# Kernel tuning notes

Measured on AMD Instinct MI355X. Metric: run time of the kernel, lower is better.

Reference implementation:

```python
import jax, jax.numpy as jnp
import numpy as np

EMBED_DIM = 1024
N_HEADS = 16

def setup_inputs() -> dict:
    key = jax.random.key(0)
    ks = jax.random.split(key, 5)
    C = EMBED_DIM
    std = 1.0 / np.sqrt(C)
    x = jax.random.normal(ks[0], (2, 2048, C), dtype=jnp.float32)
    w_attn = jax.random.normal(ks[1], (C, 3 * C), dtype=jnp.float32) * std  # (in, out)
    b_attn = jax.random.normal(ks[2], (3 * C,), dtype=jnp.float32) * 0.01
    w_proj = jax.random.normal(ks[3], (C, C), dtype=jnp.float32) * std
    b_proj = jax.random.normal(ks[4], (C,), dtype=jnp.float32) * 0.01
    return {"x": x, "w_attn": w_attn, "b_attn": b_attn, "w_proj": w_proj, "b_proj": b_proj}

def reference(x, w_attn, b_attn, w_proj, b_proj):
    B, T, C = x.shape
    H = N_HEADS
    D = C // H
    qkv = x @ w_attn + b_attn                      # (B, T, 3C)
    q, k, v = jnp.split(qkv, 3, axis=2)
    # (B, T, C) -> (B, H, T, D)
    q = q.reshape(B, T, H, D).transpose(0, 2, 1, 3)
    k = k.reshape(B, T, H, D).transpose(0, 2, 1, 3)
    v = v.reshape(B, T, H, D).transpose(0, 2, 1, 3)
    # Faithful to source: query is divided by scale BEFORE QK^T, and the
    # similarity is divided by scale AGAIN before softmax (net scale = 1/D).
    scale = jnp.asarray(D, dtype=x.dtype) ** 0.5
    q = q / scale
    sim = jnp.einsum('bhnd,bhsd->bhns', q, k)      # (B, H, T, T)
    causal = jnp.tril(jnp.ones((T, T), dtype=bool))
    neg_min = jnp.finfo(sim.dtype).min
    sim = jnp.where(causal[None, None, :, :], sim, neg_min)
    attn = jax.nn.softmax(sim / scale, axis=-1)
    out = jnp.einsum('bhns,bhsd->bhnd', attn, v)   # (B, H, T, D)
    # source: gqa returns (b n h d), forward does transpose(1,2) -> (b h n d)
    # then .view(B, T, C); net effect is reshaping the (B,H,T,D) layout.
    y = out.reshape(B, T, C)
    y = y @ w_proj + b_proj
    return y
```

## Files before the change

### kernel.cpp

```cpp
#include <hip/hip_runtime.h>
#include <hip/hip_bf16.h>

#define BB 2
#define TT 2048
#define CC 1024
#define HH 16
#define DD 64
#define MM (BB*TT)
#define QSZ ((size_t)MM*CC)

#define QSCALE 0.022542110013890053f

typedef __attribute__((ext_vector_type(8))) short bf16x8;
typedef __attribute__((ext_vector_type(4))) float f32x4;
typedef __attribute__((address_space(1))) const unsigned char as1_u8;
typedef __attribute__((address_space(3))) unsigned char as3_u8;

struct alignas(8) bf16x4_s { __hip_bfloat16 h[4]; };

static __device__ __forceinline__ unsigned cvt_pk_bf16(float lo, float hi) {
    unsigned r;
    asm("v_cvt_pk_bf16_f32 %0, %1, %2" : "=v"(r) : "v"(lo), "v"(hi));
    return r;
}

__constant__ unsigned char U_qi[48] = {
    15,31,30,31, 14,29,30,28,29, 13,27,28,26,27, 12,25,26,24,25,
    11,23,24,22,23, 10,21,22,20,21, 9,19,20,18,19, 8,17,18,16,17,
    7,16, 6,5,4,3,2,1,0};
__constant__ unsigned char U_t0[48] = {
    0,0,15,16, 0,0,0,14,15, 0,0,0,13,14, 0,0,0,12,13,
    0,0,0,11,12, 0,0,0,10,11, 0,0,0,9,10, 0,0,0,8,9,
    0,0, 0,0,0,0,0,0,0};
__constant__ unsigned char U_t1[48] = {
    16,16,31,32, 15,15,15,29,30, 14,14,14,27,28, 13,13,13,25,26,
    12,12,12,23,24, 11,11,11,21,22, 10,10,10,19,20, 9,9,9,17,18,
    8,8, 7,6,5,4,3,2,1};

__global__ __launch_bounds__(256) void prep_kernel(
    const float* __restrict__ x,  __hip_bfloat16* __restrict__ xb,
    const float* __restrict__ wa, __hip_bfloat16* __restrict__ wqkvT,
    const float* __restrict__ wp, __hip_bfloat16* __restrict__ wprojT)
{
    __shared__ float tile[64][68];
    const int t = threadIdx.x;
    const int b = blockIdx.x;
    if (b < 2048) {
        const int i = (b * 256 + t) * 8;
        const float4 a = *(const float4*)&x[i];
        const float4 c = *(const float4*)&x[i + 4];
        uint2 lo, hi;
        lo.x = cvt_pk_bf16(a.x, a.y); lo.y = cvt_pk_bf16(a.z, a.w);
        hi.x = cvt_pk_bf16(c.x, c.y); hi.y = cvt_pk_bf16(c.z, c.w);
        *(uint2*)&xb[i] = lo;
        *(uint2*)&xb[i + 4] = hi;
        return;
    }
    const float* in; __hip_bfloat16* outp; int R, Cc, bx, by;
    if (b < 2816) { const int i = b - 2048; in = wa; outp = wqkvT; R = CC; Cc = 3*CC; bx = i % 48; by = i / 48; }
    else          { const int i = b - 2816; in = wp; outp = wprojT; R = CC; Cc = CC;  bx = i % 16; by = i / 16; }
    const int c0 = bx * 64, r0 = by * 64;
    {
        const int r = t >> 2, cb = (t & 3) * 16;
        #pragma unroll
        for (int i = 0; i < 4; ++i)
            *(float4*)&tile[r][cb + i*4] = *(const float4*)&in[(size_t)(r0 + r)*Cc + c0 + cb + i*4];
    }
    __syncthreads();
    {
        const int c = t >> 2, rb = (t & 3) * 16;
        uint2 o0, o1;
        o0.x = cvt_pk_bf16(tile[rb+0][c],  tile[rb+1][c]);
        o0.y = cvt_pk_bf16(tile[rb+2][c],  tile[rb+3][c]);
        o1.x = cvt_pk_bf16(tile[rb+4][c],  tile[rb+5][c]);
        o1.y = cvt_pk_bf16(tile[rb+6][c],  tile[rb+7][c]);
        __hip_bfloat16* dst = outp + (size_t)(c0 + c)*R + r0 + rb;
        *(uint2*)&dst[0] = o0; *(uint2*)&dst[4] = o1;
        o0.x = cvt_pk_bf16(tile[rb+8][c],  tile[rb+9][c]);
        o0.y = cvt_pk_bf16(tile[rb+10][c], tile[rb+11][c]);
        o1.x = cvt_pk_bf16(tile[rb+12][c], tile[rb+13][c]);
        o1.y = cvt_pk_bf16(tile[rb+14][c], tile[rb+15][c]);
        *(uint2*)&dst[8] = o0; *(uint2*)&dst[12] = o1;
    }
}

template<int MODE>
__global__ __launch_bounds__(256) void gemm_mfma(
    const __hip_bfloat16* __restrict__ A,
    const __hip_bfloat16* __restrict__ BT,
    const float* __restrict__ bias,
    void* __restrict__ out, int M, int N, int K)
{
    __shared__ __hip_bfloat16 As[128][64];
    __shared__ __hip_bfloat16 Bs[128][64];

    const int tid = threadIdx.x;
    const int w = tid >> 6, l = tid & 63;
    const int lr = l & 15, lg = l >> 4;
    const int wr = w >> 1, wc = w & 1;
    const int rsw = (lr & 7) << 4;
    const int lsw = ((l & 7) ^ (l >> 3)) * 8;

    const int nwg = gridDim.x * gridDim.y;
    const int bid = blockIdx.y * gridDim.x + blockIdx.x;
    const int swz_id = (bid & 7) * (nwg >> 3) + (bid >> 3);
    const int row0 = (swz_id / gridDim.x) * 128;
    const int col0 = (swz_id % gridDim.x) * 128;

    f32x4 acc[4][4] = {};

    for (int k0 = 0; k0 < K; k0 += 64) {
        __syncthreads();
        #pragma unroll
        for (int i = 0; i < 4; ++i) {
            const int br = w*32 + i*8;
            const __hip_bfloat16* ga = A  + (size_t)(row0 + br + (l>>3))*K + k0 + lsw;
            __builtin_amdgcn_global_load_lds((as1_u8*)ga, (as3_u8*)&As[br][0], 16, 0, 0);
            const __hip_bfloat16* gb = BT + (size_t)(col0 + br + (l>>3))*K + k0 + lsw;
            __builtin_amdgcn_global_load_lds((as1_u8*)gb, (as3_u8*)&Bs[br][0], 16, 0, 0);
        }
        __syncthreads();

        #pragma unroll
        for (int s = 0; s < 2; ++s) {
            bf16x8 af[4], bfr[4];
            #pragma unroll
            for (int m = 0; m < 4; ++m) {
                const char* ab = (const char*)&As[wr*64 + m*16 + lr][0];
                af[m] = *(const bf16x8*)(ab + ((s*64 + lg*16) ^ rsw));
            }
            #pragma unroll
            for (int n = 0; n < 4; ++n) {
                const char* bb = (const char*)&Bs[wc*64 + n*16 + lr][0];
                bfr[n] = *(const bf16x8*)(bb + ((s*64 + lg*16) ^ rsw));
            }
            #pragma unroll
            for (int m = 0; m < 4; ++m)
                #pragma unroll
                for (int n = 0; n < 4; ++n)
                    acc[m][n] = __builtin_amdgcn_mfma_f32_16x16x32_bf16(af[m], bfr[n], acc[m][n], 0, 0, 0);
        }
    }

    #pragma unroll
    for (int m = 0; m < 4; ++m) {
        #pragma unroll
        for (int n = 0; n < 4; ++n) {
            const int ng = col0 + wc*64 + n*16 + lr;
            const float bv = bias[ng];
            const int mg0 = row0 + wr*64 + m*16 + lg*4;
            if (MODE == 0) {
                const int which = ng >> 10, c = ng & 1023;
                const int h = c >> 6, d = c & 63;
                if (which == 2) {
                    const int b = mg0 >> 11, t0 = mg0 & 2047;
                    uint2 pv;
                    pv.x = cvt_pk_bf16(acc[m][n][0] + bv, acc[m][n][1] + bv);
                    pv.y = cvt_pk_bf16(acc[m][n][2] + bv, acc[m][n][3] + bv);
                    *(uint2*)((__hip_bfloat16*)out + (size_t)2*QSZ +
                        (((size_t)(b*HH + h))*DD + d)*TT + t0) = pv;
                } else {
                    #pragma unroll
                    for (int r = 0; r < 4; ++r) {
                        const int mg = mg0 + r;
                        float v = acc[m][n][r] + bv;
                        if (which == 0) v *= QSCALE;
                        const int b = mg >> 11, t = mg & 2047;
                        ((__hip_bfloat16*)out)[(size_t)which*QSZ +
                            (((size_t)(b*HH + h))*TT + t)*DD + d] = __float2bfloat16(v);
                    }
                }
            } else {
                #pragma unroll
                for (int r = 0; r < 4; ++r)
                    ((float*)out)[(size_t)(mg0 + r)*N + ng] = acc[m][n][r] + bv;
            }
        }
    }
}

__global__ __launch_bounds__(256) void attn_mfma(
    const __hip_bfloat16* __restrict__ Qb,
    const __hip_bfloat16* __restrict__ Kb,
    const __hip_bfloat16* __restrict__ Vb,
    __hip_bfloat16* __restrict__ Ob,
    __hip_bfloat16* __restrict__ Opart,
    float* __restrict__ Lpart)
{
    __shared__ __hip_bfloat16 k_lds[64][64];
    __shared__ __hip_bfloat16 vT[64][64];
    __shared__ __hip_bfloat16 p_lds[4][16][64];

    const int tid = threadIdx.x;
    const int w  = tid >> 6;
    const int l  = tid & 63;
    const int lr = l & 15;
    const int lg = l >> 4;
    const int swz = (lr & 7) << 4;

    const int bid = blockIdx.x;
    const int sid = (bid & 7) * 192 + (bid >> 3);
    const int bh  = sid / 48;
    const int u   = sid % 48;
    const int qi  = U_qi[u];
    const int t0i = U_t0[u];
    const int t1i = U_t1[u];
    const int qb  = qi * 64;

    const __hip_bfloat16* Qh = Qb + (size_t)bh*TT*DD;
    const __hip_bfloat16* Kh = Kb + (size_t)bh*TT*DD;
    const __hip_bfloat16* Vh = Vb + (size_t)bh*DD*TT;

    bf16x8 qa[2];
    const int qrow = qb + w*16 + lr;
    {
        const __hip_bfloat16* qp = Qh + (size_t)qrow*DD + lg*8;
        qa[0] = *(const bf16x8*)(qp);
        qa[1] = *(const bf16x8*)(qp + 32);
    }

    const int off0 = (16*lg) ^ swz;
    const int off1 = (64 + 16*lg) ^ swz;
    const char* kr0b = (const char*)&k_lds[lr][0];
    const char* vr0b = (const char*)&vT[lr][0];
    char* pwb = (char*)&p_lds[w][lr][0];
    int pwo[4];
    #pragma unroll
    for (int mt = 0; mt < 4; ++mt) pwo[mt] = (32*mt + 8*lg) ^ swz;

    const int srow = tid >> 2, sch = tid & 3;
    const int wswz = (srow & 7) << 4;
    char* kwr = (char*)&k_lds[srow][0];
    char* vwr = (char*)&vT[srow][0];
    const int wo0 = (sch*32) ^ wswz, wo1 = (sch*32 + 16) ^ wswz;

    const __hip_bfloat16* ksrc = Kh + (size_t)(t0i*64 + srow)*DD + sch*16;
    const __hip_bfloat16* vsrc = Vh + (size_t)srow*TT + t0i*64 + sch*16;

    float4 kr0 = *(const float4*)ksrc, kr1 = *(const float4*)(ksrc + 8);
    float4 vr0 = *(const float4*)vsrc, vr1 = *(const float4*)(vsrc + 8);
    ksrc += 64*DD; vsrc += 64;
    *(float4*)(kwr + wo0) = kr0; *(float4*)(kwr + wo1) = kr1;
    *(float4*)(vwr + wo0) = vr0; *(float4*)(vwr + wo1) = vr1;
    __syncthreads();

    f32x4 oacc[4] = {};
    f32x4 lacc = {0.f, 0.f, 0.f, 0.f};

    for (int t = t0i; t < t1i; ++t) {
        const int kv0 = t * 64;
        const bool has_next = (t + 1 < t1i);

        if (has_next) {
            kr0 = *(const float4*)ksrc; kr1 = *(const float4*)(ksrc + 8);
            vr0 = *(const float4*)vsrc; vr1 = *(const float4*)(vsrc + 8);
            ksrc += 64*DD; vsrc += 64;
        }

        f32x4 sacc[4] = {};
        __builtin_amdgcn_s_setprio(1);
        #pragma unroll
        for (int mt = 0; mt < 4; ++mt) {
            const bf16x8 kb0 = *(const bf16x8*)(kr0b + mt*2048 + off0);
            const bf16x8 kb1 = *(const bf16x8*)(kr0b + mt*2048 + off1);
            sacc[mt] = __builtin_amdgcn_mfma_f32_16x16x32_bf16(kb0, qa[0], sacc[mt], 0, 0, 0);
            sacc[mt] = __builtin_amdgcn_mfma_f32_16x16x32_bf16(kb1, qa[1], sacc[mt], 0, 0, 0);
        }
        __builtin_amdgcn_s_setprio(0);

        if (t == qi) {
            #pragma unroll
            for (int mt = 0; mt < 4; ++mt)
                #pragma unroll
                for (int r = 0; r < 4; ++r)
                    if (kv0 + mt*16 + lg*4 + r > qrow) sacc[mt][r] = -3.0e38f;
        }
        #pragma unroll
        for (int mt = 0; mt < 4; ++mt) {
            const float p0 = exp2f(sacc[mt][0]), p1 = exp2f(sacc[mt][1]);
            const float p2 = exp2f(sacc[mt][2]), p3 = exp2f(sacc[mt][3]);
            lacc[mt] += (p0 + p1) + (p2 + p3);
            uint2 pp;
            pp.x = cvt_pk_bf16(p0, p1);
            pp.y = cvt_pk_bf16(p2, p3);
            *(uint2*)(pwb + pwo[mt]) = pp;
        }

        const bf16x8 pb0 = *(const bf16x8*)(pwb + off0);
        const bf16x8 pb1 = *(const bf16x8*)(pwb + off1);
        __builtin_amdgcn_s_setprio(1);
        #pragma unroll
        for (int dt = 0; dt < 4; ++dt) {
            const bf16x8 vb0 = *(const bf16x8*)(vr0b + dt*2048 + off0);
            const bf16x8 vb1 = *(const bf16x8*)(vr0b + dt*2048 + off1);
            oacc[dt] = __builtin_amdgcn_mfma_f32_16x16x32_bf16(vb0, pb0, oacc[dt], 0, 0, 0);
            oacc[dt] = __builtin_amdgcn_mfma_f32_16x16x32_bf16(vb1, pb1, oacc[dt], 0, 0, 0);
        }
        __builtin_amdgcn_s_setprio(0);

        if (has_next) {
            __syncthreads();
            *(float4*)(kwr + wo0) = kr0; *(float4*)(kwr + wo1) = kr1;
            *(float4*)(vwr + wo0) = vr0; *(float4*)(vwr + wo1) = vr1;
            __syncthreads();
        }
    }

    float l_r = (lacc[0] + lacc[1]) + (lacc[2] + lacc[3]);
    l_r += __shfl_xor(l_r, 16);
    l_r += __shfl_xor(l_r, 32);

    if (qi >= 16) {
        const int s = (t0i != 0);
        const int unit = ((bh*16 + (qi - 16)) << 1) | s;
        const int rowu = w*16 + lr;
        __hip_bfloat16* Oprow = Opart + ((size_t)unit*64 + rowu)*64;
        #pragma unroll
        for (int dt = 0; dt < 4; ++dt) {
            uint2 ov;
            ov.x = cvt_pk_bf16(oacc[dt][0], oacc[dt][1]);
            ov.y = cvt_pk_bf16(oacc[dt][2], oacc[dt][3]);
            *(uint2*)(Oprow + dt*16 + lg*4) = ov;
        }
        if (lg == 0) Lpart[unit*64 + rowu] = l_r;
    } else {
        __hip_bfloat16* Orow = Ob + ((size_t)bh*TT + qrow)*DD;
        const float inv = 1.0f / l_r;
        #pragma unroll
        for (int dt = 0; dt < 4; ++dt) {
            uint2 ov;
            ov.x = cvt_pk_bf16(oacc[dt][0]*inv, oacc[dt][1]*inv);
            ov.y = cvt_pk_bf16(oacc[dt][2]*inv, oacc[dt][3]*inv);
            *(uint2*)(Orow + dt*16 + lg*4) = ov;
        }
    }
}

__global__ __launch_bounds__(256) void attn_combine(
    const __hip_bfloat16* __restrict__ Opart,
    const float* __restrict__ Lpart,
    __hip_bfloat16* __restrict__ Ob)
{
    const int w = threadIdx.x >> 6, d = threadIdx.x & 63;
    const int rowg = blockIdx.x * 4 + w;
    const int r  = rowg & 63;
    const int jj = (rowg >> 6) & 15;
    const int bh = rowg >> 10;
    const int u0 = (bh*16 + jj) << 1;
    const float inv = 1.0f / (Lpart[u0*64 + r] + Lpart[(u0 + 1)*64 + r]);
    const float o1 = __bfloat162float(Opart[((size_t)u0*64 + r)*64 + d]);
    const float o2 = __bfloat162float(Opart[((size_t)(u0 + 1)*64 + r)*64 + d]);
    const int qrow = (16 + jj)*64 + r;
    Ob[((size_t)bh*TT + qrow)*DD + d] = __float2bfloat16((o1 + o2) * inv);
}

extern "C" void kernel_launch(void* const* d_in, const int* in_sizes, int n_in,
                              void* d_out, int out_size, void* d_ws, size_t ws_size,
                              hipStream_t stream)
{
    const float* x      = (const float*)d_in[0];
    const float* w_attn = (const float*)d_in[1];
    const float* b_attn = (const float*)d_in[2];
    const float* w_proj = (const float*)d_in[3];
    const float* b_proj = (const float*)d_in[4];
    float* out = (float*)d_out;

    __hip_bfloat16* xb     = (__hip_bfloat16*)d_ws;
    __hip_bfloat16* wqkvT  = xb + QSZ;
    __hip_bfloat16* wprojT = wqkvT + 3*CC*CC;
    __hip_bfloat16* Qb     = wprojT + CC*CC;
    __hip_bfloat16* Kb     = Qb + QSZ;
    __hip_bfloat16* Vt     = Kb + QSZ;
    __hip_bfloat16* Ob     = Vt + QSZ;

    __hip_bfloat16* Opart  = xb;
    float*          Lpart  = (float*)wqkvT;

    prep_kernel<<<dim3(3072), 256, 0, stream>>>(x, xb, w_attn, wqkvT, w_proj, wprojT);

    gemm_mfma<0><<<dim3(3*CC/128, MM/128), 256, 0, stream>>>(xb, wqkvT, b_attn, (void*)Qb, MM, 3*CC, CC);

    attn_mfma<<<dim3(32*48), 256, 0, stream>>>(Qb, Kb, Vt, Ob, Opart, Lpart);

    attn_combine<<<dim3(32768/4), 256, 0, stream>>>(Opart, Lpart, Ob);

    gemm_mfma<1><<<dim3(CC/128, MM/128), 256, 0, stream>>>(Ob, wprojT, b_proj, (void*)out, MM, CC, CC);
}
```

Before: 115.2 us.

## Rebalance causal attention work split into 60 units per head with 3-way splits

Changes the causal attention schedule from 48 to 60 work units per (batch, head), splitting long query tiles into two or three KV ranges of roughly equal length, about 11-12 KV tiles each. The grid mapping is changed so that 4 heads are interleaved per XCD group. The combine kernel now sums 2 or 3 partials per row and handles query tiles 12-31. This is meant to even out per-block work and improve load balance across CUs, at the cost of more partial writes and a larger combine pass.

```diff
diff --git a/kernel.cpp b/kernel.cpp
--- a/kernel.cpp
+++ b/kernel.cpp
@@ -24,18 +24,34 @@
     return r;
 }
 
-__constant__ unsigned char U_qi[48] = {
-    15,31,30,31, 14,29,30,28,29, 13,27,28,26,27, 12,25,26,24,25,
-    11,23,24,22,23, 10,21,22,20,21, 9,19,20,18,19, 8,17,18,16,17,
-    7,16, 6,5,4,3,2,1,0};
-__constant__ unsigned char U_t0[48] = {
-    0,0,15,16, 0,0,0,14,15, 0,0,0,13,14, 0,0,0,12,13,
-    0,0,0,11,12, 0,0,0,10,11, 0,0,0,9,10, 0,0,0,8,9,
-    0,0, 0,0,0,0,0,0,0};
-__constant__ unsigned char U_t1[48] = {
-    16,16,31,32, 15,15,15,29,30, 14,14,14,27,28, 13,13,13,25,26,
-    12,12,12,23,24, 11,11,11,21,22, 10,10,10,19,20, 9,9,9,17,18,
-    8,8, 7,6,5,4,3,2,1};
+__constant__ unsigned char U_qi[60] = {
+    11,22,23,23, 10,20,21,21,22,30,31,31,
+    9,18,19,19,20,27,28,28,29,29,29,30,30,31,
+    8,16,17,17,18,24,25,25,26,26,26,27,27,28,
+    7,14,15,15,16,24,24,25,
+    6,12,13,13,14,
+    5,12, 4,3,2,1,0};
+__constant__ unsigned char U_t0[60] = {
+    0,0,0,12, 0,0,0,11,12,0,0,11,
+    0,0,0,10,11,0,0,10,0,10,20,11,21,22,
+    0,0,0,9,10,0,0,9,0,9,18,10,19,20,
+    0,0,0,8,9,9,17,18,
+    0,0,0,7,8,
+    0,7, 0,0,0,0,0};
+__constant__ unsigned char U_t1[60] = {
+    12,12,12,24, 11,11,11,22,23,11,11,22,
+    10,10,10,20,21,10,10,20,10,20,30,21,31,32,
+    9,9,9,18,19,9,9,18,9,18,27,19,28,29,
+    8,8,8,16,17,17,25,26,
+    7,7,7,14,15,
+    6,13, 5,4,3,2,1};
+__constant__ unsigned char U_pu[60] = {
+    255,20,22,23, 255,16,18,19,21,42,45,46,
+    255,12,14,15,17,33,36,37,39,40,41,43,44,47,
+    255,8,10,11,13,24,27,28,30,31,32,34,35,38,
+    255,4,6,7,9,25,26,29,
+    255,0,2,3,5,
+    255,1, 255,255,255,255,255};
 
 __global__ __launch_bounds__(256) void prep_kernel(
     const float* __restrict__ x,  __hip_bfloat16* __restrict__ xb,
@@ -198,14 +214,15 @@
     const int lg = l >> 4;
     const int swz = (lr & 7) << 4;
 
-    const int bid = blockIdx.x;
-    const int sid = (bid & 7) * 192 + (bid >> 3);
-    const int bh  = sid / 48;
-    const int u   = sid % 48;
-    const int qi  = U_qi[u];
-    const int t0i = U_t0[u];
-    const int t1i = U_t1[u];
-    const int qb  = qi * 64;
+    const int bid  = blockIdx.x;
+    const int loc  = bid >> 3;
+    const int bh   = (bid & 7) * 4 + (loc & 3);
+    const int u    = loc >> 2;
+    const int qi   = U_qi[u];
+    const int t0i  = U_t0[u];
+    const int t1i  = U_t1[u];
+    const int pu   = U_pu[u];
+    const int qb   = qi * 64;
 
     const __hip_bfloat16* Qh = Qb + (size_t)bh*TT*DD;
     const __hip_bfloat16* Kh = Kb + (size_t)bh*TT*DD;
@@ -310,9 +327,8 @@
     l_r += __shfl_xor(l_r, 16);
     l_r += __shfl_xor(l_r, 32);
 
-    if (qi >= 16) {
-        const int s = (t0i != 0);
-        const int unit = ((bh*16 + (qi - 16)) << 1) | s;
+    if (pu != 255) {
+        const int unit = bh*48 + pu;
         const int rowu = w*16 + lr;
         __hip_bfloat16* Oprow = Opart + ((size_t)unit*64 + rowu)*64;
         #pragma unroll
@@ -343,15 +359,19 @@
 {
     const int w = threadIdx.x >> 6, d = threadIdx.x & 63;
     const int rowg = blockIdx.x * 4 + w;
-    const int r  = rowg & 63;
-    const int jj = (rowg >> 6) & 15;
-    const int bh = rowg >> 10;
-    const int u0 = (bh*16 + jj) << 1;
-    const float inv = 1.0f / (Lpart[u0*64 + r] + Lpart[(u0 + 1)*64 + r]);
-    const float o1 = __bfloat162float(Opart[((size_t)u0*64 + r)*64 + d]);
-    const float o2 = __bfloat162float(Opart[((size_t)(u0 + 1)*64 + r)*64 + d]);
-    const int qrow = (16 + jj)*64 + r;
-    Ob[((size_t)bh*TT + qrow)*DD + d] = __float2bfloat16((o1 + o2) * inv);
+    const int bh  = rowg / 1280;
+    const int rem = rowg - bh * 1280;
+    const int spb = rem >> 6;
+    const int r   = rem & 63;
+    const int nu  = (spb < 12) ? 2 : 3;
+    const int pu0 = bh*48 + ((spb < 12) ? 2*spb : 24 + 3*(spb - 12));
+    float o = 0.f, lsum = 0.f;
+    for (int i = 0; i < nu; ++i) {
+        o    += __bfloat162float(Opart[((size_t)(pu0 + i)*64 + r)*64 + d]);
+        lsum += Lpart[(pu0 + i)*64 + r];
+    }
+    const int qrow = (12 + spb)*64 + r;
+    Ob[((size_t)bh*TT + qrow)*DD + d] = __float2bfloat16(o / lsum);
 }
 
 extern "C" void kernel_launch(void* const* d_in, const int* in_sizes, int n_in,
@@ -374,15 +394,15 @@
     __hip_bfloat16* Ob     = Vt + QSZ;
 
     __hip_bfloat16* Opart  = xb;
-    float*          Lpart  = (float*)wqkvT;
+    float*          Lpart  = (float*)(xb + (size_t)1536*64*64);
 
     prep_kernel<<<dim3(3072), 256, 0, stream>>>(x, xb, w_attn, wqkvT, w_proj, wprojT);
 
     gemm_mfma<0><<<dim3(3*CC/128, MM/128), 256, 0, stream>>>(xb, wqkvT, b_attn, (void*)Qb, MM, 3*CC, CC);
 
-    attn_mfma<<<dim3(32*48), 256, 0, stream>>>(Qb, Kb, Vt, Ob, Opart, Lpart);
-
-    attn_combine<<<dim3(32768/4), 256, 0, stream>>>(Opart, Lpart, Ob);
+    attn_mfma<<<dim3(1920), 256, 0, stream>>>(Qb, Kb, Vt, Ob, Opart, Lpart);
+
+    attn_combine<<<dim3(40960/4), 256, 0, stream>>>(Opart, Lpart, Ob);
 
     gemm_mfma<1><<<dim3(CC/128, MM/128), 256, 0, stream>>>(Ob, wprojT, b_proj, (void*)out, MM, CC, CC);
 }
```

New measurement: 114.6 us. No clear change (-0.5%).
